# Optimization experiments

Measured on AMD Instinct MI355X. Metric: run time of the kernel, lower is better.

The kernel has to match this reference:

```python
import jax, jax.numpy as jnp
import numpy as np

D_IN = 1024
D_OUT = 1024
N_HEADS = 16
D_H = D_OUT // N_HEADS


def setup_inputs() -> dict:
    key = jax.random.key(0)
    k_x, k_q, k_k, k_v = jax.random.split(key, 4)
    x = jax.random.normal(k_x, (4, 2048, D_IN), dtype=jnp.float32)
    s = 1.0 / np.sqrt(D_IN)
    # weights stored as [d_in, d_out] (transpose of torch Linear.weight)
    W_q = jax.random.uniform(k_q, (D_IN, D_OUT), dtype=jnp.float32, minval=-s, maxval=s)
    W_k = jax.random.uniform(k_k, (D_IN, D_OUT), dtype=jnp.float32, minval=-s, maxval=s)
    W_v = jax.random.uniform(k_v, (D_IN, D_OUT), dtype=jnp.float32, minval=-s, maxval=s)
    return {"x": x, "W_q": W_q, "W_k": W_k, "W_v": W_v}


def reference(x, W_q, W_k, W_v):
    B, T, _ = x.shape
    # QKV projections -> [B, H, T, d_h]
    def split_heads(y):
        return y.reshape(B, T, N_HEADS, D_H).transpose(0, 2, 1, 3)
    q = split_heads(x @ W_q)
    k = split_heads(x @ W_k)
    v = split_heads(x @ W_v)
    # attention scores [B, H, T, T]
    scores = jnp.einsum('bhqd,bhkd->bhqk', q, k)
    causal = jnp.tril(jnp.ones((T, T), dtype=bool))  # True = keep
    scores = jnp.where(causal, scores, -jnp.inf)
    weights = jax.nn.softmax(scores / np.sqrt(D_H), axis=-1)
    ctx = jnp.einsum('bhqk,bhkd->bhqd', weights, v)  # [B,H,T,d_h]
    return ctx.transpose(0, 2, 1, 3).reshape(B, T, D_OUT)
```

## Files before the change

kernel.cpp:

```cpp
#include <hip/hip_runtime.h>
#include <stdint.h>

typedef float f32x4 __attribute__((ext_vector_type(4)));
typedef __bf16 bf16x8 __attribute__((ext_vector_type(8)));

#define LOG2E 1.4426950408889634f
#define SCL2 (0.125f * LOG2E)

static __device__ __forceinline__ unsigned short f2bf(float f) {
  unsigned int u = __builtin_bit_cast(unsigned int, f);
  u += 0x7fffu + ((u >> 16) & 1u);
  return (unsigned short)(u >> 16);
}

static __device__ __forceinline__ void gload16(const void* g, void* l) {
  __builtin_amdgcn_global_load_lds(
      (const __attribute__((address_space(1))) unsigned int*)g,
      (__attribute__((address_space(3))) unsigned int*)l, 16, 0, 0);
}

__global__ void prep_kernel(const float* __restrict__ x, const float* __restrict__ Wq,
                            const float* __restrict__ Wk, const float* __restrict__ Wv,
                            unsigned short* __restrict__ xb, unsigned short* __restrict__ Wt) {
  __shared__ float t[32][33];
  if (blockIdx.x < 4096) {
    size_t i = ((size_t)blockIdx.x * 256 + threadIdx.x) * 8;
    const float4 a = *(const float4*)(x + i);
    const float4 b = *(const float4*)(x + i + 4);
    union { unsigned short us[8]; uint4 u; } o;
    o.us[0] = f2bf(a.x); o.us[1] = f2bf(a.y); o.us[2] = f2bf(a.z); o.us[3] = f2bf(a.w);
    o.us[4] = f2bf(b.x); o.us[5] = f2bf(b.y); o.us[6] = f2bf(b.z); o.us[7] = f2bf(b.w);
    *(uint4*)(xb + i) = o.u;
  } else {
    const int b = blockIdx.x - 4096;
    const int z = b >> 10;
    const int rem = b & 1023;
    const float* W = (z == 0) ? Wq : ((z == 1) ? Wk : Wv);
    unsigned short* o = Wt + (size_t)z * 1048576;
    const int k0 = (rem >> 5) * 32, n0 = (rem & 31) * 32;
    const int tx = threadIdx.x & 31, ty = threadIdx.x >> 5;
#pragma unroll
    for (int i = 0; i < 4; ++i)
      t[ty + i * 8][tx] = W[(size_t)(k0 + ty + i * 8) * 1024 + n0 + tx];
    __syncthreads();
#pragma unroll
    for (int i = 0; i < 4; ++i)
      o[(size_t)(n0 + ty + i * 8) * 1024 + k0 + tx] = f2bf(t[tx][ty + i * 8]);
  }
}

__global__ __launch_bounds__(256) void gemm_qkv(
    const unsigned short* __restrict__ xb, const unsigned short* __restrict__ Wt,
    unsigned short* __restrict__ Qb, unsigned short* __restrict__ Kb,
    unsigned short* __restrict__ Vtb) {
  __shared__ uint4 ldsab[2048];
  char* ldsc = (char*)ldsab;
  const int tid = threadIdx.x;
  const int lane = tid & 63;
  const int li = lane & 15, g = lane >> 4;
  const int wv = tid >> 6, wr = wv >> 1, wc = wv & 1;
  const int L = blockIdx.x;
  const int W = (L & 7) * 192 + (L >> 3);
  const int z = W >> 9;
  const int rem = W & 511;
  const int m0 = (rem >> 3) * 128, n0 = (rem & 7) * 128;
  const char* Abase = (const char*)xb;
  const char* Bbase = (const char*)(Wt + (size_t)z * 1048576);

  const f32x4 fz = {0.f, 0.f, 0.f, 0.f};
  f32x4 acc[4][4];
#pragma unroll
  for (int m = 0; m < 4; ++m)
#pragma unroll
    for (int n = 0; n < 4; ++n) acc[m][n] = fz;

  for (int kt = 0; kt < 16; ++kt) {
    __syncthreads();
#pragma unroll
    for (int i = 0; i < 4; ++i) {
      const int c = i * 256 + tid, r = c >> 3, cr = c & 7;
      gload16(Abase + (size_t)(m0 + r) * 2048 + kt * 128 + ((cr ^ (r & 7)) * 16),
              ldsc + c * 16);
      gload16(Bbase + (size_t)(n0 + r) * 2048 + kt * 128 + ((cr ^ (r & 7)) * 16),
              ldsc + 16384 + c * 16);
    }
    __syncthreads();
#pragma unroll
    for (int ks = 0; ks < 2; ++ks) {
      bf16x8 a[4], b[4];
#pragma unroll
      for (int m = 0; m < 4; ++m) {
        const int ra = wr * 64 + m * 16 + li;
        a[m] = *(const bf16x8*)(ldsc + ra * 128 + (((ks * 4 + g) ^ (ra & 7)) * 16));
      }
#pragma unroll
      for (int n = 0; n < 4; ++n) {
        const int rb = wc * 64 + n * 16 + li;
        b[n] = *(const bf16x8*)(ldsc + 16384 + rb * 128 + (((ks * 4 + g) ^ (rb & 7)) * 16));
      }
#pragma unroll
      for (int m = 0; m < 4; ++m)
#pragma unroll
        for (int n = 0; n < 4; ++n)
          acc[m][n] = __builtin_amdgcn_mfma_f32_16x16x32_bf16(a[m], b[n], acc[m][n], 0, 0, 0);
    }
  }

  __syncthreads();
  char* tb = ldsc + wv * 8192;
  if (z == 2) {
#pragma unroll
    for (int m = 0; m < 4; ++m)
#pragma unroll
      for (int n = 0; n < 4; ++n) {
        const int d_l = n * 16 + li;
#pragma unroll
        for (int rp = 0; rp < 2; ++rp) {
          const int t_l = m * 16 + g * 4 + rp * 2;
          const int t5 = t_l & 31;
          const int ks2 = t_l >> 5;
          const int rr = t5 & 15;
          const int gp = ((rr >> 3) & 1) * 2 + ((rr >> 2) & 1);
          const int j = (t5 & 3) + ((t5 >> 4) << 2);
          const unsigned lo = f2bf(acc[m][n][rp * 2]);
          const unsigned hi2 = f2bf(acc[m][n][rp * 2 + 1]);
          *(unsigned*)(tb + d_l * 128 + (((ks2 * 4 + gp) ^ (d_l & 7)) * 16) + j * 2) =
              lo | (hi2 << 16);
        }
      }
    __syncthreads();
    const int t0g = m0 + wr * 64;
    const int bI2 = t0g >> 11, tt2 = t0g & 2047;
    const int hh = (n0 + wc * 64) >> 6;
#pragma unroll
    for (int p2 = 0; p2 < 8; ++p2) {
      const int d_l = p2 * 8 + (lane >> 3);
      const int c8 = lane & 7;
      const uint4 v = *(const uint4*)(tb + d_l * 128 + ((c8 ^ (d_l & 7)) * 16));
      *(uint4*)((char*)Vtb +
                ((((size_t)(bI2 * 16 + hh) * 64 + d_l) * 2048 + tt2 + c8 * 8) * 2)) = v;
    }
  } else {
    const float sc = (z == 0) ? SCL2 : 1.0f;
#pragma unroll
    for (int m = 0; m < 4; ++m)
#pragma unroll
      for (int n = 0; n < 4; ++n) {
        const int ch = n * 2 + (li >> 3);
        const int eo = (li & 7) * 2;
#pragma unroll
        for (int r = 0; r < 4; ++r) {
          const int t_l = m * 16 + g * 4 + r;
          *(unsigned short*)(tb + t_l * 128 + ((ch ^ (t_l & 7)) * 16) + eo) =
              f2bf(acc[m][n][r] * sc);
        }
      }
    __syncthreads();
    const int t0g = m0 + wr * 64;
    const int bI = t0g >> 11, tt = t0g & 2047;
    const int h = (n0 + wc * 64) >> 6;
    unsigned short* dst = ((z == 0) ? Qb : Kb) + ((size_t)(bI * 16 + h) * 2048 + tt) * 64;
#pragma unroll
    for (int p = 0; p < 8; ++p) {
      const int t_l = p * 8 + (lane >> 3);
      const int c8 = lane & 7;
      const uint4 v = *(const uint4*)(tb + t_l * 128 + ((c8 ^ (t_l & 7)) * 16));
      *(uint4*)((char*)dst + t_l * 128 + c8 * 16) = v;
    }
  }
}

__global__ __launch_bounds__(512, 4) void attn_kernel(
    const unsigned short* __restrict__ Qb, const unsigned short* __restrict__ Kb,
    const unsigned short* __restrict__ Vtb, float* __restrict__ out) {
  __shared__ uint4 lds[4096];
  char* ldsc = (char*)lds;
  const int L = blockIdx.x;
  const int W = (L & 7) * 64 + (L >> 3);
  const int bh = W >> 3;
  const int qp = W & 7;
  const int tid = threadIdx.x;
  const int lane = tid & 63, wv = tid >> 6;
  const int grp = wv >> 2, wq = wv & 3;
  const int t256 = tid & 255;
  const int li = lane & 15, g = lane >> 4;

  char* gbase = ldsc + grp * 32768;

  const char* Qrow = (const char*)Qb + (size_t)bh * 2048 * 128;
  const char* Krow = (const char*)Kb + (size_t)bh * 2048 * 128;
  const char* Vrow = (const char*)Vtb + (size_t)bh * 64 * 4096;
  const int bI = bh >> 4, h = bh & 15;
  const f32x4 fz = {0.f, 0.f, 0.f, 0.f};

  union { unsigned int u[4]; bf16x8 v; } onesu;
  onesu.u[0] = 0x3F803F80u; onesu.u[1] = 0x3F803F80u;
  onesu.u[2] = 0x3F803F80u; onesu.u[3] = 0x3F803F80u;
  const bf16x8 ones = onesu.v;

  auto stage = [&](int b, int kt) {
#pragma unroll
    for (int i = 0; i < 2; ++i) {
      const int c = i * 256 + t256, r = c >> 3, cr = c & 7;
      gload16(Krow + (size_t)(kt * 64 + r) * 128 + ((cr ^ (r & 7)) * 16),
              gbase + b * 16384 + c * 16);
      gload16(Vrow + (size_t)r * 4096 + kt * 128 + ((cr ^ (r & 7)) * 16),
              gbase + b * 16384 + 8192 + c * 16);
    }
  };

  for (int half = 0; half < 2; ++half) {
    const int qt = half ? (15 - qp) : qp;
    const int q0 = qt * 128;
    const int qw = q0 + wq * 32;
    const int hc = qt + 1;
    const int kbeg = grp ? hc : 0;

    uint4 qf[2][2];
#pragma unroll
    for (int nq = 0; nq < 2; ++nq)
#pragma unroll
      for (int ks = 0; ks < 2; ++ks)
        qf[nq][ks] = *(const uint4*)(Qrow + (size_t)(qw + nq * 16 + li) * 128 + ks * 64 + g * 16);

    float mrow[2] = {-1e30f, -1e30f};
    float lrow[2] = {0.0f, 0.0f};
    f32x4 lsum[2] = {fz, fz};
    f32x4 ctx[4][2];
#pragma unroll
    for (int mtd = 0; mtd < 4; ++mtd)
#pragma unroll
      for (int nq = 0; nq < 2; ++nq) ctx[mtd][nq] = fz;

    stage(0, kbeg);

    for (int it = 0; it < hc; ++it) {
      const int kt = kbeg + it;
      __syncthreads();
      if (it + 1 < hc) stage((it + 1) & 1, kt + 1);
      if (kt * 64 > qw + 31) continue;

      const char* sK = gbase + (it & 1) * 16384;
      const char* sV = sK + 8192;

      f32x4 st[4][2];
#pragma unroll
      for (int mt = 0; mt < 4; ++mt)
#pragma unroll
        for (int nq = 0; nq < 2; ++nq) st[mt][nq] = fz;
      __builtin_amdgcn_s_setprio(1);
#pragma unroll
      for (int ks = 0; ks < 2; ++ks) {
        bf16x8 kf[4];
#pragma unroll
        for (int mt = 0; mt < 4; ++mt) {
          const int rk = mt * 16 + li;
          kf[mt] = *(const bf16x8*)(sK + rk * 128 + (((ks * 4 + g) ^ (rk & 7)) * 16));
        }
#pragma unroll
        for (int mt = 0; mt < 4; ++mt)
#pragma unroll
          for (int nq = 0; nq < 2; ++nq)
            st[mt][nq] = __builtin_amdgcn_mfma_f32_16x16x32_bf16(
                kf[mt], __builtin_bit_cast(bf16x8, qf[nq][ks]), st[mt][nq], 0, 0, 0);
      }
      __builtin_amdgcn_s_setprio(0);

      const bool full = (kt * 64 + 63 <= qw);
      bf16x8 pb[2][2];
#pragma unroll
      for (int nq = 0; nq < 2; ++nq) {
        float p[4][4];
        if (full) {
#pragma unroll
          for (int mt = 0; mt < 4; ++mt)
#pragma unroll
            for (int r = 0; r < 4; ++r) p[mt][r] = st[mt][nq][r];
        } else {
          const int qg_ = qw + nq * 16 + li;
#pragma unroll
          for (int mt = 0; mt < 4; ++mt)
#pragma unroll
            for (int r = 0; r < 4; ++r)
              p[mt][r] = (kt * 64 + mt * 16 + g * 4 + r > qg_) ? -__builtin_inff()
                                                               : st[mt][nq][r];
        }
        const float m1 = fmaxf(fmaxf(p[0][0], p[0][1]), p[0][2]);
        const float m2 = fmaxf(fmaxf(p[0][3], p[1][0]), p[1][1]);
        const float m3 = fmaxf(fmaxf(p[1][2], p[1][3]), p[2][0]);
        const float m4 = fmaxf(fmaxf(p[2][1], p[2][2]), p[2][3]);
        const float m5 = fmaxf(fmaxf(p[3][0], p[3][1]), p[3][2]);
        const float lmax = fmaxf(fmaxf(fmaxf(m1, m2), m3), fmaxf(fmaxf(m4, m5), p[3][3]));
        if (!__all(lmax <= mrow[nq] + 8.0f)) {
          float tmax = fmaxf(lmax, __shfl_xor(lmax, 16, 64));
          tmax = fmaxf(tmax, __shfl_xor(tmax, 32, 64));
          const float mnew = fmaxf(mrow[nq], tmax);
          const float resc = __builtin_amdgcn_exp2f(mrow[nq] - mnew);
          mrow[nq] = mnew;
          lsum[nq] = lsum[nq] * resc;
#pragma unroll
          for (int mtd = 0; mtd < 4; ++mtd) ctx[mtd][nq] = ctx[mtd][nq] * resc;
        }
        const float mcur = mrow[nq];
#pragma unroll
        for (int mt = 0; mt < 4; ++mt)
#pragma unroll
          for (int r = 0; r < 4; ++r)
            p[mt][r] = __builtin_amdgcn_exp2f(p[mt][r] - mcur);
#pragma unroll
        for (int ks2 = 0; ks2 < 2; ++ks2) {
          union { __bf16 b[8]; bf16x8 v; } u;
#pragma unroll
          for (int r = 0; r < 4; ++r) {
            u.b[r] = (__bf16)p[2 * ks2][r];
            u.b[4 + r] = (__bf16)p[2 * ks2 + 1][r];
          }
          pb[nq][ks2] = u.v;
        }
      }

      __builtin_amdgcn_s_setprio(1);
#pragma unroll
      for (int ks2 = 0; ks2 < 2; ++ks2) {
#pragma unroll
        for (int mtd = 0; mtd < 4; ++mtd) {
          const int rd = mtd * 16 + li;
          const bf16x8 vf =
              *(const bf16x8*)(sV + rd * 128 + (((ks2 * 4 + g) ^ (rd & 7)) * 16));
#pragma unroll
          for (int nq = 0; nq < 2; ++nq)
            ctx[mtd][nq] = __builtin_amdgcn_mfma_f32_16x16x32_bf16(vf, pb[nq][ks2], ctx[mtd][nq], 0, 0, 0);
        }
#pragma unroll
        for (int nq = 0; nq < 2; ++nq)
          lsum[nq] = __builtin_amdgcn_mfma_f32_16x16x32_bf16(ones, pb[nq][ks2], lsum[nq], 0, 0, 0);
      }
      __builtin_amdgcn_s_setprio(0);
    }

    lrow[0] = lsum[0][0];
    lrow[1] = lsum[1][0];

    __syncthreads();
    if (grp == 1) {
      char* mb = ldsc + 32768;
#pragma unroll
      for (int nqp = 0; nqp < 2; ++nqp)
#pragma unroll
        for (int mtd = 0; mtd < 4; ++mtd)
          *(f32x4*)(mb + (wq * 64 + lane) * 128 + nqp * 64 + ((mtd ^ (lane & 3)) * 16)) = ctx[mtd][nqp];
      if (g == 0) {
#pragma unroll
        for (int nqp = 0; nqp < 2; ++nqp) {
          ((float*)ldsc)[nqp * 64 + wq * 16 + li] = mrow[nqp];
          ((float*)(ldsc + 512))[nqp * 64 + wq * 16 + li] = lrow[nqp];
        }
      }
    }
    __syncthreads();
    if (grp == 0) {
      const char* mb = ldsc + 32768;
#pragma unroll
      for (int nqp = 0; nqp < 2; ++nqp) {
        const float mB = ((const float*)ldsc)[nqp * 64 + wq * 16 + li];
        const float lB = ((const float*)(ldsc + 512))[nqp * 64 + wq * 16 + li];
        const float mM = fmaxf(mrow[nqp], mB);
        const float cA = __builtin_amdgcn_exp2f(mrow[nqp] - mM);
        const float cB = __builtin_amdgcn_exp2f(mB - mM);
        const float inv = 1.0f / (lrow[nqp] * cA + lB * cB);
        const float fA = cA * inv, fB = cB * inv;
#pragma unroll
        for (int mtd = 0; mtd < 4; ++mtd) {
          const f32x4 cb = *(const f32x4*)(mb + (wq * 64 + lane) * 128 + nqp * 64 + ((mtd ^ (lane & 3)) * 16));
          ctx[mtd][nqp] = ctx[mtd][nqp] * fA + cb * fB;
        }
      }
    }
    __syncthreads();

    if (grp == 0) {
      float* trb = (float*)(ldsc + wq * 8192);
#pragma unroll
      for (int nqp = 0; nqp < 2; ++nqp)
#pragma unroll
        for (int mtd = 0; mtd < 4; ++mtd)
#pragma unroll
          for (int r = 0; r < 4; ++r) {
            const int q = nqp * 16 + li;
            const int d = mtd * 16 + g * 4 + r;
            trb[q * 64 + ((((d >> 2) ^ (q & 15)) << 2) | (d & 3))] = ctx[mtd][nqp][r];
          }
    }
    __syncthreads();
    if (grp == 0) {
      const float* trb = (const float*)(ldsc + wq * 8192);
#pragma unroll
      for (int pass = 0; pass < 8; ++pass) {
        const int qr = pass * 4 + g;
        const float4 v = *(const float4*)&trb[qr * 64 + ((li ^ (qr & 15)) << 2)];
        *(float4*)(out + ((size_t)bI * 2048 + q0 + wq * 32 + qr) * 1024 + h * 64 + li * 4) = v;
      }
    }
    __syncthreads();
  }
}

extern "C" void kernel_launch(void* const* d_in, const int* in_sizes, int n_in,
                              void* d_out, int out_size, void* d_ws, size_t ws_size,
                              hipStream_t stream) {
  (void)in_sizes; (void)n_in; (void)out_size; (void)ws_size;
  const float* x  = (const float*)d_in[0];
  const float* Wq = (const float*)d_in[1];
  const float* Wk = (const float*)d_in[2];
  const float* Wv = (const float*)d_in[3];
  float* out = (float*)d_out;
  char* ws = (char*)d_ws;
  unsigned short* xb  = (unsigned short*)ws;
  unsigned short* Wt  = (unsigned short*)(ws + 16777216);
  unsigned short* Qb  = (unsigned short*)(ws + 23068672);
  unsigned short* Kb  = (unsigned short*)(ws + 39845888);
  unsigned short* Vtb = (unsigned short*)(ws + 56623104);

  hipLaunchKernelGGL(prep_kernel, dim3(4096 + 3072), dim3(256), 0, stream,
                     x, Wq, Wk, Wv, xb, Wt);
  hipLaunchKernelGGL(gemm_qkv, dim3(1536), dim3(256), 0, stream, xb, Wt, Qb, Kb, Vtb);
  hipLaunchKernelGGL(attn_kernel, dim3(512), dim3(512), 0, stream, Qb, Kb, Vtb, out);
}
```

Baseline: 165.1 us.

## Software-pipeline QK^T of next tile with PV of previous tile in attention

Restructures the attention inner loop so each iteration computes the QK^T scores and softmax for the current key tile while issuing the PV MFMAs for the previous tile's probabilities. K is double-buffered and V is triple-buffered in LDS so V data stays alive one extra iteration, and LDS grows from 64KB to 80KB per block. The aim is to overlap the exp/softmax VALU work with MFMA work and shorten dependency stalls. The cost is more LDS per block, which may reduce occupancy, plus an extra loop iteration with conditional branches.

```diff
diff --git a/kernel.cpp b/kernel.cpp
--- a/kernel.cpp
+++ b/kernel.cpp
@@ -173,7 +173,7 @@
 __global__ __launch_bounds__(512, 4) void attn_kernel(
     const unsigned short* __restrict__ Qb, const unsigned short* __restrict__ Kb,
     const unsigned short* __restrict__ Vtb, float* __restrict__ out) {
-  __shared__ uint4 lds[4096];
+  __shared__ uint4 lds[5120];
   char* ldsc = (char*)lds;
   const int L = blockIdx.x;
   const int W = (L & 7) * 64 + (L >> 3);
@@ -185,7 +185,7 @@
   const int t256 = tid & 255;
   const int li = lane & 15, g = lane >> 4;
 
-  char* gbase = ldsc + grp * 32768;
+  char* gbase = ldsc + grp * 40960;
 
   const char* Qrow = (const char*)Qb + (size_t)bh * 2048 * 128;
   const char* Krow = (const char*)Kb + (size_t)bh * 2048 * 128;
@@ -198,14 +198,14 @@
   onesu.u[2] = 0x3F803F80u; onesu.u[3] = 0x3F803F80u;
   const bf16x8 ones = onesu.v;
 
-  auto stage = [&](int b, int kt) {
+  auto stage = [&](int t) {
+    char* kb = gbase + (t & 1) * 8192;
+    char* vb = gbase + 16384 + (t % 3) * 8192;
 #pragma unroll
     for (int i = 0; i < 2; ++i) {
       const int c = i * 256 + t256, r = c >> 3, cr = c & 7;
-      gload16(Krow + (size_t)(kt * 64 + r) * 128 + ((cr ^ (r & 7)) * 16),
-              gbase + b * 16384 + c * 16);
-      gload16(Vrow + (size_t)r * 4096 + kt * 128 + ((cr ^ (r & 7)) * 16),
-              gbase + b * 16384 + 8192 + c * 16);
+      gload16(Krow + (size_t)(t * 64 + r) * 128 + ((cr ^ (r & 7)) * 16), kb + c * 16);
+      gload16(Vrow + (size_t)r * 4096 + t * 128 + ((cr ^ (r & 7)) * 16), vb + c * 16);
     }
   };
 
@@ -232,110 +232,117 @@
 #pragma unroll
       for (int nq = 0; nq < 2; ++nq) ctx[mtd][nq] = fz;
 
-    stage(0, kbeg);
-
-    for (int it = 0; it < hc; ++it) {
-      const int kt = kbeg + it;
+    bf16x8 pb[2][2];
+
+    stage(kbeg);
+
+    for (int r = 0; r <= hc; ++r) {
+      const int cur = kbeg + r;
       __syncthreads();
-      if (it + 1 < hc) stage((it + 1) & 1, kt + 1);
-      if (kt * 64 > qw + 31) continue;
-
-      const char* sK = gbase + (it & 1) * 16384;
-      const char* sV = sK + 8192;
+      if (r + 1 < hc) stage(kbeg + r + 1);
+      const bool doQ = (r < hc) && (cur * 64 <= qw + 31);
+      const bool doP = (r >= 1) && ((cur - 1) * 64 <= qw + 31);
 
       f32x4 st[4][2];
-#pragma unroll
-      for (int mt = 0; mt < 4; ++mt)
-#pragma unroll
-        for (int nq = 0; nq < 2; ++nq) st[mt][nq] = fz;
-      __builtin_amdgcn_s_setprio(1);
-#pragma unroll
-      for (int ks = 0; ks < 2; ++ks) {
-        bf16x8 kf[4];
-#pragma unroll
-        for (int mt = 0; mt < 4; ++mt) {
-          const int rk = mt * 16 + li;
-          kf[mt] = *(const bf16x8*)(sK + rk * 128 + (((ks * 4 + g) ^ (rk & 7)) * 16));
-        }
+      if (doQ) {
+        const char* sK = gbase + (cur & 1) * 8192;
 #pragma unroll
         for (int mt = 0; mt < 4; ++mt)
 #pragma unroll
+          for (int nq = 0; nq < 2; ++nq) st[mt][nq] = fz;
+        __builtin_amdgcn_s_setprio(1);
+#pragma unroll
+        for (int ks = 0; ks < 2; ++ks) {
+          bf16x8 kf[4];
+#pragma unroll
+          for (int mt = 0; mt < 4; ++mt) {
+            const int rk = mt * 16 + li;
+            kf[mt] = *(const bf16x8*)(sK + rk * 128 + (((ks * 4 + g) ^ (rk & 7)) * 16));
+          }
+#pragma unroll
+          for (int mt = 0; mt < 4; ++mt)
+#pragma unroll
+            for (int nq = 0; nq < 2; ++nq)
+              st[mt][nq] = __builtin_amdgcn_mfma_f32_16x16x32_bf16(
+                  kf[mt], __builtin_bit_cast(bf16x8, qf[nq][ks]), st[mt][nq], 0, 0, 0);
+        }
+        __builtin_amdgcn_s_setprio(0);
+      }
+
+      if (doP) {
+        const char* sV = gbase + 16384 + ((cur - 1) % 3) * 8192;
+        __builtin_amdgcn_s_setprio(1);
+#pragma unroll
+        for (int ks2 = 0; ks2 < 2; ++ks2) {
+#pragma unroll
+          for (int mtd = 0; mtd < 4; ++mtd) {
+            const int rd = mtd * 16 + li;
+            const bf16x8 vf =
+                *(const bf16x8*)(sV + rd * 128 + (((ks2 * 4 + g) ^ (rd & 7)) * 16));
+#pragma unroll
+            for (int nq = 0; nq < 2; ++nq)
+              ctx[mtd][nq] = __builtin_amdgcn_mfma_f32_16x16x32_bf16(vf, pb[nq][ks2], ctx[mtd][nq], 0, 0, 0);
+          }
+#pragma unroll
           for (int nq = 0; nq < 2; ++nq)
-            st[mt][nq] = __builtin_amdgcn_mfma_f32_16x16x32_bf16(
-                kf[mt], __builtin_bit_cast(bf16x8, qf[nq][ks]), st[mt][nq], 0, 0, 0);
-      }
-      __builtin_amdgcn_s_setprio(0);
-
-      const bool full = (kt * 64 + 63 <= qw);
-      bf16x8 pb[2][2];
-#pragma unroll
-      for (int nq = 0; nq < 2; ++nq) {
-        float p[4][4];
-        if (full) {
+            lsum[nq] = __builtin_amdgcn_mfma_f32_16x16x32_bf16(ones, pb[nq][ks2], lsum[nq], 0, 0, 0);
+        }
+        __builtin_amdgcn_s_setprio(0);
+      }
+
+      if (doQ) {
+        const bool full = (cur * 64 + 63 <= qw);
+#pragma unroll
+        for (int nq = 0; nq < 2; ++nq) {
+          float p[4][4];
+          if (full) {
+#pragma unroll
+            for (int mt = 0; mt < 4; ++mt)
+#pragma unroll
+              for (int r2 = 0; r2 < 4; ++r2) p[mt][r2] = st[mt][nq][r2];
+          } else {
+            const int qg_ = qw + nq * 16 + li;
+#pragma unroll
+            for (int mt = 0; mt < 4; ++mt)
+#pragma unroll
+              for (int r2 = 0; r2 < 4; ++r2)
+                p[mt][r2] = (cur * 64 + mt * 16 + g * 4 + r2 > qg_) ? -__builtin_inff()
+                                                                    : st[mt][nq][r2];
+          }
+          const float m1 = fmaxf(fmaxf(p[0][0], p[0][1]), p[0][2]);
+          const float m2 = fmaxf(fmaxf(p[0][3], p[1][0]), p[1][1]);
+          const float m3 = fmaxf(fmaxf(p[1][2], p[1][3]), p[2][0]);
+          const float m4 = fmaxf(fmaxf(p[2][1], p[2][2]), p[2][3]);
+          const float m5 = fmaxf(fmaxf(p[3][0], p[3][1]), p[3][2]);
+          const float lmax = fmaxf(fmaxf(fmaxf(m1, m2), m3), fmaxf(fmaxf(m4, m5), p[3][3]));
+          if (!__all(lmax <= mrow[nq] + 8.0f)) {
+            float tmax = fmaxf(lmax, __shfl_xor(lmax, 16, 64));
+            tmax = fmaxf(tmax, __shfl_xor(tmax, 32, 64));
+            const float mnew = fmaxf(mrow[nq], tmax);
+            const float resc = __builtin_amdgcn_exp2f(mrow[nq] - mnew);
+            mrow[nq] = mnew;
+            lsum[nq] = lsum[nq] * resc;
+#pragma unroll
+            for (int mtd = 0; mtd < 4; ++mtd) ctx[mtd][nq] = ctx[mtd][nq] * resc;
+          }
+          const float mcur = mrow[nq];
 #pragma unroll
           for (int mt = 0; mt < 4; ++mt)
 #pragma unroll
-            for (int r = 0; r < 4; ++r) p[mt][r] = st[mt][nq][r];
-        } else {
-          const int qg_ = qw + nq * 16 + li;
-#pragma unroll
-          for (int mt = 0; mt < 4; ++mt)
-#pragma unroll
-            for (int r = 0; r < 4; ++r)
-              p[mt][r] = (kt * 64 + mt * 16 + g * 4 + r > qg_) ? -__builtin_inff()
-                                                               : st[mt][nq][r];
-        }
-        const float m1 = fmaxf(fmaxf(p[0][0], p[0][1]), p[0][2]);
-        const float m2 = fmaxf(fmaxf(p[0][3], p[1][0]), p[1][1]);
-        const float m3 = fmaxf(fmaxf(p[1][2], p[1][3]), p[2][0]);
-        const float m4 = fmaxf(fmaxf(p[2][1], p[2][2]), p[2][3]);
-        const float m5 = fmaxf(fmaxf(p[3][0], p[3][1]), p[3][2]);
-        const float lmax = fmaxf(fmaxf(fmaxf(m1, m2), m3), fmaxf(fmaxf(m4, m5), p[3][3]));
-        if (!__all(lmax <= mrow[nq] + 8.0f)) {
-          float tmax = fmaxf(lmax, __shfl_xor(lmax, 16, 64));
-          tmax = fmaxf(tmax, __shfl_xor(tmax, 32, 64));
-          const float mnew = fmaxf(mrow[nq], tmax);
-          const float resc = __builtin_amdgcn_exp2f(mrow[nq] - mnew);
-          mrow[nq] = mnew;
-          lsum[nq] = lsum[nq] * resc;
-#pragma unroll
-          for (int mtd = 0; mtd < 4; ++mtd) ctx[mtd][nq] = ctx[mtd][nq] * resc;
-        }
-        const float mcur = mrow[nq];
-#pragma unroll
-        for (int mt = 0; mt < 4; ++mt)
-#pragma unroll
-          for (int r = 0; r < 4; ++r)
-            p[mt][r] = __builtin_amdgcn_exp2f(p[mt][r] - mcur);
-#pragma unroll
-        for (int ks2 = 0; ks2 < 2; ++ks2) {
-          union { __bf16 b[8]; bf16x8 v; } u;
-#pragma unroll
-          for (int r = 0; r < 4; ++r) {
-            u.b[r] = (__bf16)p[2 * ks2][r];
-            u.b[4 + r] = (__bf16)p[2 * ks2 + 1][r];
-          }
-          pb[nq][ks2] = u.v;
-        }
-      }
-
-      __builtin_amdgcn_s_setprio(1);
-#pragma unroll
-      for (int ks2 = 0; ks2 < 2; ++ks2) {
-#pragma unroll
-        for (int mtd = 0; mtd < 4; ++mtd) {
-          const int rd = mtd * 16 + li;
-          const bf16x8 vf =
-              *(const bf16x8*)(sV + rd * 128 + (((ks2 * 4 + g) ^ (rd & 7)) * 16));
-#pragma unroll
-          for (int nq = 0; nq < 2; ++nq)
-            ctx[mtd][nq] = __builtin_amdgcn_mfma_f32_16x16x32_bf16(vf, pb[nq][ks2], ctx[mtd][nq], 0, 0, 0);
-        }
-#pragma unroll
-        for (int nq = 0; nq < 2; ++nq)
-          lsum[nq] = __builtin_amdgcn_mfma_f32_16x16x32_bf16(ones, pb[nq][ks2], lsum[nq], 0, 0, 0);
-      }
-      __builtin_amdgcn_s_setprio(0);
+            for (int r2 = 0; r2 < 4; ++r2)
+              p[mt][r2] = __builtin_amdgcn_exp2f(p[mt][r2] - mcur);
+#pragma unroll
+          for (int ks2 = 0; ks2 < 2; ++ks2) {
+            union { __bf16 b[8]; bf16x8 v; } u;
+#pragma unroll
+            for (int r2 = 0; r2 < 4; ++r2) {
+              u.b[r2] = (__bf16)p[2 * ks2][r2];
+              u.b[4 + r2] = (__bf16)p[2 * ks2 + 1][r2];
+            }
+            pb[nq][ks2] = u.v;
+          }
+        }
+      }
     }
 
     lrow[0] = lsum[0][0];
@@ -343,7 +350,7 @@
 
     __syncthreads();
     if (grp == 1) {
-      char* mb = ldsc + 32768;
+      char* mb = ldsc + 40960;
 #pragma unroll
       for (int nqp = 0; nqp < 2; ++nqp)
 #pragma unroll
@@ -359,7 +366,7 @@
     }
     __syncthreads();
     if (grp == 0) {
-      const char* mb = ldsc + 32768;
+      const char* mb = ldsc + 40960;
 #pragma unroll
       for (int nqp = 0; nqp < 2; ++nqp) {
         const float mB = ((const float*)ldsc)[nqp * 64 + wq * 16 + li];
@@ -385,10 +392,10 @@
 #pragma unroll
         for (int mtd = 0; mtd < 4; ++mtd)
 #pragma unroll
-          for (int r = 0; r < 4; ++r) {
+          for (int r2 = 0; r2 < 4; ++r2) {
             const int q = nqp * 16 + li;
-            const int d = mtd * 16 + g * 4 + r;
-            trb[q * 64 + ((((d >> 2) ^ (q & 15)) << 2) | (d & 3))] = ctx[mtd][nqp][r];
+            const int d = mtd * 16 + g * 4 + r2;
+            trb[q * 64 + ((((d >> 2) ^ (q & 15)) << 2) | (d & 3))] = ctx[mtd][nqp][r2];
           }
     }
     __syncthreads();
```

Result: slower. 331.1 us (+100.6%).
